# Kernel tuning notes

Measured on AMD Instinct MI355X. Metric: run time of the kernel, lower is better.

Reference implementation:

```python
import jax, jax.numpy as jnp
import numpy as np

WS = 16  # window_size

def _conv1x1(x, w, b):
    # x: [n,c,h,w], w: [out,in], b: [out]
    return jnp.einsum('nchw,oc->nohw', x, w) + b[None, :, None, None]

def _se_attention(x, w1, b1, w2, b2):
    # global avg pool -> conv -> relu -> conv -> sigmoid; returns [n,C,1,1]
    p = x.mean(axis=(2, 3), keepdims=True)
    h = jax.nn.relu(_conv1x1(p, w1, b1))
    return jax.nn.sigmoid(_conv1x1(h, w2, b2))

def setup_inputs() -> dict:
    key = jax.random.key(0)
    ks = jax.random.split(key, 13)
    B, C, H, W = 8, 96, 256, 256
    Cr = C // 3
    s = 0.02
    return {
        'x': jax.random.normal(ks[0], (B, C, H, W), jnp.float32),
        'w_real': jax.random.normal(ks[1], (C, C), jnp.float32) * s,
        'b_real': jnp.zeros((C,), jnp.float32),
        'w_imag': jax.random.normal(ks[2], (C, C), jnp.float32) * s,
        'b_imag': jnp.zeros((C,), jnp.float32),
        'car_w1': jax.random.normal(ks[3], (Cr, C), jnp.float32) * s,
        'car_b1': jnp.zeros((Cr,), jnp.float32),
        'car_w2': jax.random.normal(ks[4], (C, Cr), jnp.float32) * s,
        'car_b2': jnp.zeros((C,), jnp.float32),
        'cai_w1': jax.random.normal(ks[5], (Cr, C), jnp.float32) * s,
        'cai_b1': jnp.zeros((Cr,), jnp.float32),
        'cai_w2': jax.random.normal(ks[6], (C, Cr), jnp.float32) * s,
        'cai_b2': jnp.zeros((C,), jnp.float32),
    }

def reference(x, w_real, b_real, w_imag, b_imag,
              car_w1, car_b1, car_w2, car_b2,
              cai_w1, cai_b1, cai_w2, cai_b2):
    B, C, H, W = x.shape
    nH, nW = H // WS, W // WS
    # window partition: [B,C,H,W] -> [B*nH*nW, C, WS, WS]
    xw = x.reshape(B, C, nH, WS, nW, WS)
    xw = xw.transpose(0, 2, 4, 1, 3, 5).reshape(-1, C, WS, WS)
    # 2D FFT per window, ortho norm
    x_fft = jnp.fft.fft2(xw, norm='ortho')
    real_conv = _conv1x1(jnp.real(x_fft), w_real, b_real)
    imag_conv = _conv1x1(jnp.imag(x_fft), w_imag, b_imag)
    real_att = _se_attention(real_conv, car_w1, car_b1, car_w2, car_b2)
    imag_att = _se_attention(imag_conv, cai_w1, cai_b1, cai_w2, cai_b2)
    real_conv = real_conv * (1.0 + real_att)
    imag_conv = imag_conv * (1.0 + imag_att)
    x_fft_enh = jax.lax.complex(real_conv, imag_conv)
    x_ifft = jnp.real(jnp.fft.ifft2(x_fft_enh, norm='ortho'))
    # window merge: [B*nH*nW, C, WS, WS] -> [B,C,H,W]
    out = x_ifft.reshape(B, nH, nW, C, WS, WS)
    out = out.transpose(0, 3, 1, 4, 2, 5).reshape(B, C, H, W)
    return out
```

## Files before the change

kernel.cpp:

```cpp
#include <hip/hip_runtime.h>
#include <hip/hip_bf16.h>
#include <math.h>

#define NWIN 2048

typedef __bf16 v8bf __attribute__((ext_vector_type(8)));
typedef __bf16 v2bf __attribute__((ext_vector_type(2)));
typedef float  v4f  __attribute__((ext_vector_type(4)));

__global__ __launch_bounds__(128) void se_alpha_kernel(
    const float* __restrict__ x,
    const float* __restrict__ w_real, const float* __restrict__ b_real,
    const float* __restrict__ car_w1, const float* __restrict__ car_b1,
    const float* __restrict__ car_w2, const float* __restrict__ car_b2,
    const float* __restrict__ b_imag,
    const float* __restrict__ cai_w1, const float* __restrict__ cai_b1,
    const float* __restrict__ cai_w2, const float* __restrict__ cai_b2,
    float* __restrict__ alpha, float* __restrict__ beta)
{
    __shared__ float wr_s[96 * 97];
    __shared__ float vec_s[96];
    __shared__ float pr_s[96];
    __shared__ float h1_s[32];
    const int t = threadIdx.x;
    const int n = blockIdx.x;

    if (n < NWIN) {
        const int b = n >> 8, wh = (n >> 4) & 15, ww = n & 15;
        for (int idx = t; idx < 96 * 96; idx += 128) {
            int o = idx / 96;
            int c = idx - o * 96;
            wr_s[o * 97 + c] = w_real[idx];
        }
        if (t < 96)
            vec_s[t] = x[(((size_t)(b * 96 + t)) * 256 + wh * 16) * 256 + ww * 16];
        __syncthreads();
        if (t < 96) {
            float acc = 0.f;
            #pragma unroll 8
            for (int c = 0; c < 96; ++c) acc += wr_s[t * 97 + c] * vec_s[c];
            pr_s[t] = acc * (1.0f / 16.0f) + b_real[t];
        }
        __syncthreads();
        if (t < 32) {
            float acc = car_b1[t];
            for (int o = 0; o < 96; ++o) acc += car_w1[t * 96 + o] * pr_s[o];
            h1_s[t] = fmaxf(acc, 0.f);
        }
        __syncthreads();
        if (t < 96) {
            float acc = car_b2[t];
            for (int j = 0; j < 32; ++j) acc += car_w2[t * 32 + j] * h1_s[j];
            alpha[n * 96 + t] = 1.f + 1.f / (1.f + __expf(-acc));
        }
    } else {
        if (t < 32) {
            float acc = cai_b1[t];
            for (int o = 0; o < 96; ++o) acc += cai_w1[t * 96 + o] * b_imag[o];
            h1_s[t] = fmaxf(acc, 0.f);
        }
        __syncthreads();
        if (t < 96) {
            float acc = cai_b2[t];
            for (int j = 0; j < 32; ++j) acc += cai_w2[t * 32 + j] * h1_s[j];
            beta[t] = 1.f + 1.f / (1.f + __expf(-acc));
        }
    }
}

__global__ __launch_bounds__(256, 2) void wfca_main_kernel(
    const float* __restrict__ x,
    const float* __restrict__ w_real, const float* __restrict__ w_imag,
    const float* __restrict__ b_real,
    const float* __restrict__ alpha, const float* __restrict__ beta,
    float* __restrict__ out)
{
    __shared__ __bf16 x_lds[256 * 40];
    __shared__ __bf16 w1_lds[96 * 40];
    __shared__ __bf16 w2_lds[96 * 40];

    const int t = threadIdx.x;
    const int nwin = blockIdx.x;
    const int b = nwin >> 8, wh = (nwin >> 4) & 15, ww = nwin & 15;
    const int lane = t & 63;
    const int wave = t >> 6;
    const int l16 = lane & 15;
    const int quad = lane >> 4;

    const int sw = t & 15;
    const int scp = t >> 4;
    const int wc = t & 31;
    const int wo0 = t >> 5;

    v4f acc[4][6];
    #pragma unroll
    for (int i = 0; i < 4; ++i)
        #pragma unroll
        for (int j = 0; j < 6; ++j)
            acc[i][j] = v4f{0.f, 0.f, 0.f, 0.f};

    const size_t xbase = (((size_t)b * 96) * 256 + wh * 16) * 256 + ww * 16;

    for (int kc = 0; kc < 3; ++kc) {
        const int c0 = kc * 32;
        if (kc) __syncthreads();

        {
            const float* xp = x + xbase + (size_t)(c0 + 2 * scp) * 65536 + sw;
            #pragma unroll
            for (int h = 0; h < 16; ++h) {
                float f0 = xp[h * 256];
                float f1 = xp[h * 256 + 65536];
                v2bf pk;
                pk[0] = (__bf16)f0;
                pk[1] = (__bf16)f1;
                *(v2bf*)&x_lds[(h * 16 + sw) * 40 + 2 * scp] = pk;
            }
        }
        {
            #pragma unroll
            for (int i = 0; i < 12; ++i) {
                int o = wo0 + 8 * i;
                float wr = w_real[o * 96 + c0 + wc];
                float wi = w_imag[o * 96 + c0 + wc];
                float a  = alpha[nwin * 96 + o];
                float bt = beta[o];
                w1_lds[o * 40 + wc] = (__bf16)(0.5f * (a * wr + bt * wi));
                w2_lds[o * 40 + wc] = (__bf16)(0.5f * (a * wr - bt * wi));
            }
        }
        __syncthreads();

        v8bf a_x[4], a_f[4];
        #pragma unroll
        for (int mi = 0; mi < 4; ++mi) {
            int h = wave * 4 + mi;
            a_x[mi] = *(const v8bf*)&x_lds[(h * 16 + l16) * 40 + quad * 8];
            int hf = (16 - h) & 15;
            int wf = (16 - l16) & 15;
            a_f[mi] = *(const v8bf*)&x_lds[(hf * 16 + wf) * 40 + quad * 8];
        }
        #pragma unroll
        for (int n = 0; n < 6; ++n) {
            v8bf b1 = *(const v8bf*)&w1_lds[(n * 16 + l16) * 40 + quad * 8];
            v8bf b2 = *(const v8bf*)&w2_lds[(n * 16 + l16) * 40 + quad * 8];
            #pragma unroll
            for (int mi = 0; mi < 4; ++mi) {
                acc[mi][n] = __builtin_amdgcn_mfma_f32_16x16x32_bf16(a_x[mi], b1, acc[mi][n], 0, 0, 0);
                acc[mi][n] = __builtin_amdgcn_mfma_f32_16x16x32_bf16(a_f[mi], b2, acc[mi][n], 0, 0, 0);
            }
        }
    }

    #pragma unroll
    for (int n = 0; n < 6; ++n) {
        int o = n * 16 + l16;
        #pragma unroll
        for (int mi = 0; mi < 4; ++mi) {
            int h = wave * 4 + mi;
            v4f v = acc[mi][n];
            if (h == 0 && quad == 0) {
                v[0] += 16.f * alpha[nwin * 96 + o] * b_real[o];
            }
            size_t idx = (((size_t)(b * 96 + o)) * 256 + wh * 16 + h) * 256 + ww * 16 + quad * 4;
            *(v4f*)(out + idx) = v;
        }
    }
}

extern "C" void kernel_launch(void* const* d_in, const int* in_sizes, int n_in,
                              void* d_out, int out_size, void* d_ws, size_t ws_size,
                              hipStream_t stream) {
    const float* x      = (const float*)d_in[0];
    const float* w_real = (const float*)d_in[1];
    const float* b_real = (const float*)d_in[2];
    const float* w_imag = (const float*)d_in[3];
    const float* b_imag = (const float*)d_in[4];
    const float* car_w1 = (const float*)d_in[5];
    const float* car_b1 = (const float*)d_in[6];
    const float* car_w2 = (const float*)d_in[7];
    const float* car_b2 = (const float*)d_in[8];
    const float* cai_w1 = (const float*)d_in[9];
    const float* cai_b1 = (const float*)d_in[10];
    const float* cai_w2 = (const float*)d_in[11];
    const float* cai_b2 = (const float*)d_in[12];
    float* out = (float*)d_out;

    float* alpha = (float*)d_ws;
    float* beta  = alpha + NWIN * 96;

    se_alpha_kernel<<<NWIN + 1, 128, 0, stream>>>(
        x, w_real, b_real, car_w1, car_b1, car_w2, car_b2,
        b_imag, cai_w1, cai_b1, cai_w2, cai_b2, alpha, beta);

    wfca_main_kernel<<<NWIN, 256, 0, stream>>>(
        x, w_real, w_imag, b_real, alpha, beta, out);
}
```

Before: 429.5 us.

## Process eight windows per block with double-buffered LDS staging and shared weights

The main kernel now uses 1024-thread blocks that each handle eight consecutive windows. The per-window alpha scaling moves out of the weight matrix and into the epilogue, so the bf16 real and imag weights are built once per block and stay in LDS. Global loads for the next channel chunk are issued before the current chunk's MFMAs and written into a second LDS buffer, overlapping load latency with compute. The cost is twice as many MFMAs per output, since U and V are accumulated separately. Only 256 blocks are launched, which may underfill the GPU, and each thread holds more registers.

```diff
diff --git a/kernel.cpp b/kernel.cpp
--- a/kernel.cpp
+++ b/kernel.cpp
@@ -7,6 +7,7 @@
 typedef __bf16 v8bf __attribute__((ext_vector_type(8)));
 typedef __bf16 v2bf __attribute__((ext_vector_type(2)));
 typedef float  v4f  __attribute__((ext_vector_type(4)));
+typedef unsigned int v4u __attribute__((ext_vector_type(4)));
 
 __global__ __launch_bounds__(128) void se_alpha_kernel(
     const float* __restrict__ x,
@@ -68,102 +69,128 @@
     }
 }
 
-__global__ __launch_bounds__(256, 2) void wfca_main_kernel(
+__global__ __launch_bounds__(1024, 4) void wfca_main_kernel(
     const float* __restrict__ x,
     const float* __restrict__ w_real, const float* __restrict__ w_imag,
     const float* __restrict__ b_real,
     const float* __restrict__ alpha, const float* __restrict__ beta,
     float* __restrict__ out)
 {
-    __shared__ __bf16 x_lds[256 * 40];
-    __shared__ __bf16 w1_lds[96 * 40];
-    __shared__ __bf16 w2_lds[96 * 40];
-
-    const int t = threadIdx.x;
-    const int nwin = blockIdx.x;
-    const int b = nwin >> 8, wh = (nwin >> 4) & 15, ww = nwin & 15;
+    __shared__ __bf16 wr_s[96 * 104];
+    __shared__ __bf16 wi_s[96 * 104];
+    __shared__ __bf16 x_lds[2][256 * 40];
+
+    const int t    = threadIdx.x;
+    const int blk  = blockIdx.x;
+    const int b    = blk >> 5;
+    const int wh   = (blk >> 1) & 15;
+    const int ww0  = (blk & 1) * 8;
+
     const int lane = t & 63;
-    const int wave = t >> 6;
-    const int l16 = lane & 15;
+    const int l16  = lane & 15;
     const int quad = lane >> 4;
-
-    const int sw = t & 15;
-    const int scp = t >> 4;
-    const int wc = t & 31;
-    const int wo0 = t >> 5;
-
-    v4f acc[4][6];
+    const int wv   = t >> 6;
+
+    const int sw  = t & 15;
+    const int scp = (t >> 4) & 15;
+    const int hq  = t >> 8;
+
+    const float* xb = x + (((size_t)(b * 96)) << 16) + (size_t)(wh * 16) * 256;
+
+    float st0[4], st1[4];
+
+    auto stage_issue = [&](int win_, int k_) {
+        const float* xp = xb + (((size_t)(k_ * 32 + 2 * scp)) << 16)
+                             + (ww0 + win_) * 16 + sw;
+        #pragma unroll
+        for (int r = 0; r < 4; ++r) {
+            int h = hq * 4 + r;
+            st0[r] = xp[h * 256];
+            st1[r] = xp[h * 256 + 65536];
+        }
+    };
+    auto stage_write = [&](int bufsel) {
+        #pragma unroll
+        for (int r = 0; r < 4; ++r) {
+            int h = hq * 4 + r;
+            v2bf pk;
+            pk[0] = (__bf16)st0[r];
+            pk[1] = (__bf16)st1[r];
+            *(v2bf*)&x_lds[bufsel][(h * 16 + sw) * 40 + 2 * scp] = pk;
+        }
+    };
+
+    stage_issue(0, 0);
+    float wrv[9], wiv[9], btv[9];
     #pragma unroll
-    for (int i = 0; i < 4; ++i)
-        #pragma unroll
-        for (int j = 0; j < 6; ++j)
-            acc[i][j] = v4f{0.f, 0.f, 0.f, 0.f};
-
-    const size_t xbase = (((size_t)b * 96) * 256 + wh * 16) * 256 + ww * 16;
-
-    for (int kc = 0; kc < 3; ++kc) {
-        const int c0 = kc * 32;
-        if (kc) __syncthreads();
-
-        {
-            const float* xp = x + xbase + (size_t)(c0 + 2 * scp) * 65536 + sw;
-            #pragma unroll
-            for (int h = 0; h < 16; ++h) {
-                float f0 = xp[h * 256];
-                float f1 = xp[h * 256 + 65536];
-                v2bf pk;
-                pk[0] = (__bf16)f0;
-                pk[1] = (__bf16)f1;
-                *(v2bf*)&x_lds[(h * 16 + sw) * 40 + 2 * scp] = pk;
-            }
-        }
-        {
-            #pragma unroll
-            for (int i = 0; i < 12; ++i) {
-                int o = wo0 + 8 * i;
-                float wr = w_real[o * 96 + c0 + wc];
-                float wi = w_imag[o * 96 + c0 + wc];
-                float a  = alpha[nwin * 96 + o];
-                float bt = beta[o];
-                w1_lds[o * 40 + wc] = (__bf16)(0.5f * (a * wr + bt * wi));
-                w2_lds[o * 40 + wc] = (__bf16)(0.5f * (a * wr - bt * wi));
-            }
-        }
-        __syncthreads();
-
-        v8bf a_x[4], a_f[4];
-        #pragma unroll
-        for (int mi = 0; mi < 4; ++mi) {
-            int h = wave * 4 + mi;
-            a_x[mi] = *(const v8bf*)&x_lds[(h * 16 + l16) * 40 + quad * 8];
-            int hf = (16 - h) & 15;
-            int wf = (16 - l16) & 15;
-            a_f[mi] = *(const v8bf*)&x_lds[(hf * 16 + wf) * 40 + quad * 8];
-        }
+    for (int r = 0; r < 9; ++r) {
+        int idx = t + r * 1024;
+        wrv[r] = w_real[idx];
+        wiv[r] = w_imag[idx];
+        btv[r] = beta[idx / 96];
+    }
+    float brv[6];
+    #pragma unroll
+    for (int n = 0; n < 6; ++n) brv[n] = b_real[n * 16 + l16];
+    #pragma unroll
+    for (int r = 0; r < 9; ++r) {
+        int idx = t + r * 1024;
+        int o = idx / 96, c = idx - o * 96;
+        wr_s[o * 104 + c] = (__bf16)(0.5f * wrv[r]);
+        wi_s[o * 104 + c] = (__bf16)(0.5f * btv[r] * wiv[r]);
+    }
+    stage_write(0);
+    __syncthreads();
+
+    v4f U[6], V[6];
+    int cur = 0;
+    for (int win = 0; win < 8; ++win) {
+        float af[6];
         #pragma unroll
         for (int n = 0; n < 6; ++n) {
-            v8bf b1 = *(const v8bf*)&w1_lds[(n * 16 + l16) * 40 + quad * 8];
-            v8bf b2 = *(const v8bf*)&w2_lds[(n * 16 + l16) * 40 + quad * 8];
+            af[n] = alpha[(size_t)(blk * 8 + win) * 96 + n * 16 + l16];
+            U[n] = v4f{0.f, 0.f, 0.f, 0.f};
+            V[n] = v4f{0.f, 0.f, 0.f, 0.f};
+        }
+        for (int k = 0; k < 3; ++k) {
+            const bool last = (win == 7 && k == 2);
+            if (!last) stage_issue(k == 2 ? win + 1 : win, k == 2 ? 0 : k + 1);
+
+            const __bf16* xl = x_lds[cur];
+            v8bf a_x = *(const v8bf*)&xl[(wv * 16 + l16) * 40 + quad * 8];
+            const int hf = (16 - wv) & 15, wf = (16 - l16) & 15;
+            v8bf a_f = *(const v8bf*)&xl[(hf * 16 + wf) * 40 + quad * 8];
+            v4u fu = __builtin_bit_cast(v4u, a_f);
+            const v4u sm = {0x80008000u, 0x80008000u, 0x80008000u, 0x80008000u};
+            v8bf a_fn = __builtin_bit_cast(v8bf, fu ^ sm);
+
+            const int c0 = k * 32;
             #pragma unroll
-            for (int mi = 0; mi < 4; ++mi) {
-                acc[mi][n] = __builtin_amdgcn_mfma_f32_16x16x32_bf16(a_x[mi], b1, acc[mi][n], 0, 0, 0);
-                acc[mi][n] = __builtin_amdgcn_mfma_f32_16x16x32_bf16(a_f[mi], b2, acc[mi][n], 0, 0, 0);
+            for (int n = 0; n < 6; ++n) {
+                v8bf bwr = *(const v8bf*)&wr_s[(n * 16 + l16) * 104 + c0 + quad * 8];
+                v8bf bwi = *(const v8bf*)&wi_s[(n * 16 + l16) * 104 + c0 + quad * 8];
+                U[n] = __builtin_amdgcn_mfma_f32_16x16x32_bf16(a_x,  bwr, U[n], 0, 0, 0);
+                U[n] = __builtin_amdgcn_mfma_f32_16x16x32_bf16(a_f,  bwr, U[n], 0, 0, 0);
+                V[n] = __builtin_amdgcn_mfma_f32_16x16x32_bf16(a_x,  bwi, V[n], 0, 0, 0);
+                V[n] = __builtin_amdgcn_mfma_f32_16x16x32_bf16(a_fn, bwi, V[n], 0, 0, 0);
             }
-        }
-    }
-
-    #pragma unroll
-    for (int n = 0; n < 6; ++n) {
-        int o = n * 16 + l16;
-        #pragma unroll
-        for (int mi = 0; mi < 4; ++mi) {
-            int h = wave * 4 + mi;
-            v4f v = acc[mi][n];
-            if (h == 0 && quad == 0) {
-                v[0] += 16.f * alpha[nwin * 96 + o] * b_real[o];
+            if (k == 2) {
+                const int col = (ww0 + win) * 16;
+                #pragma unroll
+                for (int n = 0; n < 6; ++n) {
+                    const int o = n * 16 + l16;
+                    v4f v;
+                    #pragma unroll
+                    for (int r = 0; r < 4; ++r) v[r] = af[n] * U[n][r] + V[n][r];
+                    if (wv == 0 && quad == 0) v[0] += 16.f * af[n] * brv[n];
+                    size_t idx = (((size_t)(b * 96 + o)) * 256 + wh * 16 + wv) * 256
+                                 + col + quad * 4;
+                    *(v4f*)(out + idx) = v;
+                }
             }
-            size_t idx = (((size_t)(b * 96 + o)) * 256 + wh * 16 + h) * 256 + ww * 16 + quad * 4;
-            *(v4f*)(out + idx) = v;
+            if (!last) stage_write(cur ^ 1);
+            __syncthreads();
+            cur ^= 1;
         }
     }
 }
@@ -193,6 +220,6 @@
         x, w_real, b_real, car_w1, car_b1, car_w2, car_b2,
         b_imag, cai_w1, cai_b1, cai_w2, cai_b2, alpha, beta);
 
-    wfca_main_kernel<<<NWIN, 256, 0, stream>>>(
+    wfca_main_kernel<<<256, 1024, 0, stream>>>(
         x, w_real, w_imag, b_real, alpha, beta, out);
 }
```

Result: slower. 454.7 us (+5.9%).
